# Kernel tuning notes

Hardware: AMD Instinct MI355X
Metric: run time of the kernel (lower is better)

## Reference

```python
import jax, jax.numpy as jnp
import numpy as np

N, F, E = 65536, 64, 16   # batch, fields, embedding_size
H1, H2 = 8, 4             # hidden_dims
BN_EPS = 1e-5


def setup_inputs() -> dict:
    key = jax.random.key(0)
    ks = jax.random.split(key, 12)
    rn = lambda k, shape, sc=1.0: jax.random.normal(k, shape, dtype=jnp.float32) * sc
    return {
        "Xa": rn(ks[0], (N, F)),
        "Xc": rn(ks[1], (N, F)),
        # per-field Linear(1,1) weights/biases (two first-order embedding lists)
        "w1": rn(ks[2], (F,)), "b1": rn(ks[3], (F,)),
        "w2": rn(ks[4], (F,)), "b2": rn(ks[5], (F,)),
        # per-field Linear(1,E) weights/biases (two second-order embedding lists)
        "W1": rn(ks[6], (F, E)), "B1": rn(ks[7], (F, E)),
        "W2": rn(ks[8], (F, E)), "B2": rn(ks[9], (F, E)),
        # deep MLP: linear_1 (F*E -> 8) + BN, linear_2 (8 -> 4). No final layer (init bug).
        "lin1_w": rn(ks[10], (H1, F * E), 0.01), "lin1_b": jnp.zeros((H1,), jnp.float32),
        "bn1_gamma": jnp.ones((H1,), jnp.float32), "bn1_beta": jnp.zeros((H1,), jnp.float32),
        "lin2_w": rn(ks[11], (H2, H1), 0.01), "lin2_b": jnp.full((H2,), 0.21, jnp.float32),
    }


def reference(Xa, Xc, w1, b1, w2, b2, W1, B1, W2, B2,
              lin1_w, lin1_b, bn1_gamma, bn1_beta, lin2_w, lin2_b):
    n = Xa.shape[0]
    # ---- FM first order (faithful to the torch broadcast: arr_2[i] is (N,N)
    # with entry [r,c] = Xa[r,i]*(w2[i]*Xc[c,i]+b2[i]); only mean over the
    # concat dim is consumed, so compute the column-mean analytically). ----
    first1 = (w1 * Xa + b1) * Xc                         # (N,F)
    xc_mean = jnp.mean(Xc, axis=0)                       # (F,)
    first2_cmean = Xa * (w2 * xc_mean + b2)              # (N,F) = mean over c of arr_2
    fm_first_mean = jnp.mean(first1 + first2_cmean, axis=1, keepdims=True)  # (N,1)

    # ---- FM second order: per-field (N,E) embeddings, fully batched. ----
    Xa3 = Xa[:, :, None]                                 # (N,F,1)
    Xc3 = Xc[:, :, None]
    emb = (Xa3 * W1 + B1) * Xc3 + Xa3 * (W2 * Xc3 + B2)  # (N,F,E)
    s = emb.sum(axis=1)                                  # (N,E)
    fm_second = 0.5 * (s * s - (emb * emb).sum(axis=1))  # (N,E)
    fm_second_mean = jnp.mean(fm_second, axis=1, keepdims=True)  # (N,1)

    # ---- deep part: cat of per-field (N,E) -> (N, F*E), field-major. ----
    deep = emb.reshape(n, F * E)
    h = deep @ lin1_w.T + lin1_b                         # (N,8)
    mu = h.mean(axis=0)
    var = h.var(axis=0)                                  # biased, as BN training mode
    h = (h - mu) / jnp.sqrt(var + BN_EPS) * bn1_gamma + bn1_beta
    h = jnp.tanh(h)                                      # dropout = identity (eval)
    h = h @ lin2_w.T + lin2_b                            # (N,4) — no final projection (init bug)
    deep_mean = h.mean(axis=1, keepdims=True)            # (N,1)

    return fm_first_mean + fm_second_mean + deep_mean    # (N,1)
```

## Files before the change

kernel.cpp:

```cpp
#include <hip/hip_runtime.h>
#include <math.h>

#define NROWS 65536
#define BN_EPS 1e-5f
#define MBLK   512
#define TSTR   1024

#define OFF_PARTIAL 0
#define OFF_H       65536
#define OFF_REC     589824
#define OFF_BLKT    595200
#define OFF_T       677120

__global__ __launch_bounds__(64) void precompute_kernel(
    const float* __restrict__ W1, const float* __restrict__ B1,
    const float* __restrict__ W2, const float* __restrict__ B2,
    const float* __restrict__ lin1_w, const float* __restrict__ w1,
    const float* __restrict__ b1, const float* __restrict__ b2,
    float* __restrict__ rec)
{
    int f = blockIdx.x, t = threadIdx.x;
    __shared__ float u[16], x[16], y[16];
    if (t < 16) {
        float uu = W1[f * 16 + t] + W2[f * 16 + t];
        float xx = B1[f * 16 + t];
        float yy = B2[f * 16 + t];
        u[t] = uu; x[t] = xx; y[t] = yy;
        rec[f * 84 + t]      = uu;
        rec[f * 84 + 16 + t] = xx;
        rec[f * 84 + 32 + t] = yy;
    }
    __syncthreads();
    if (t < 24) {
        int j = t & 7, which = t >> 3;
        const float* src = (which == 0) ? u : (which == 1) ? x : y;
        const float* lw = lin1_w + j * 1024 + f * 16;
        float acc = 0.f;
#pragma unroll
        for (int e = 0; e < 16; e++) acc = fmaf(src[e], lw[e], acc);
        rec[f * 84 + 48 + which * 8 + j] = acc;
    } else if (t < 30) {
        int q = t - 24;
        const float* s1 = (q == 0 || q == 3 || q == 4) ? u : (q == 1 || q == 5) ? x : y;
        const float* s2 = (q == 0) ? u : (q == 1 || q == 3) ? x : y;
        float acc = 0.f;
#pragma unroll
        for (int e = 0; e < 16; e++) acc = fmaf(s1[e], s2[e], acc);
        rec[f * 84 + 72 + q] = (q < 3 ? 1.f : 2.f) * acc;
    } else if (t == 30) {
        rec[f * 84 + 78] = w1[f];
        rec[f * 84 + 79] = b1[f];
        rec[f * 84 + 80] = b2[f];
        rec[f * 84 + 81] = 0.f;
        rec[f * 84 + 82] = 0.f;
        rec[f * 84 + 83] = 0.f;
    }
}

__global__ __launch_bounds__(256)
__attribute__((amdgpu_waves_per_eu(2, 4)))
void main_kernel(
    const float* __restrict__ Xa, const float* __restrict__ Xc,
    const float* __restrict__ rec, const float* __restrict__ lin1_b,
    float* __restrict__ ws_partial, float* __restrict__ ws_h,
    float* __restrict__ ws_blkT)
{
    __shared__ __align__(16) float smem[14848];

    int tid  = threadIdx.x;
    int lane = tid & 63;
    int wv   = tid >> 6;
    int wu   = __builtin_amdgcn_readfirstlane(wv);
    int blk  = blockIdx.x;
    int f0   = wu * 16;
    int row0 = blk * 128 + lane;
    int row1 = row0 + 64;

    {
        const float4* src = (const float4*)rec;
        float4* dst = (float4*)smem;
        for (int i = tid; i < 1344; i += 256) dst[i] = src[i];
    }

    const float4* pa0 = (const float4*)(Xa + (size_t)row0 * 64 + f0);
    const float4* pc0 = (const float4*)(Xc + (size_t)row0 * 64 + f0);
    const float4* pa1 = (const float4*)(Xa + (size_t)row1 * 64 + f0);
    const float4* pc1 = (const float4*)(Xc + (size_t)row1 * 64 + f0);
    float a_[16], c_[16], a2_[16], c2_[16];
#pragma unroll
    for (int k = 0; k < 4; k++) {
        float4 av = pa0[k], cv = pc0[k];
        a_[k * 4] = av.x; a_[k * 4 + 1] = av.y; a_[k * 4 + 2] = av.z; a_[k * 4 + 3] = av.w;
        c_[k * 4] = cv.x; c_[k * 4 + 1] = cv.y; c_[k * 4 + 2] = cv.z; c_[k * 4 + 3] = cv.w;
        float4 av2 = pa1[k], cv2 = pc1[k];
        a2_[k * 4] = av2.x; a2_[k * 4 + 1] = av2.y; a2_[k * 4 + 2] = av2.z; a2_[k * 4 + 3] = av2.w;
        c2_[k * 4] = cv2.x; c2_[k * 4 + 1] = cv2.y; c2_[k * 4 + 2] = cv2.z; c2_[k * 4 + 3] = cv2.w;
    }
    __syncthreads();

    float s[16], s2[16], hh[8], hh2[8];
#pragma unroll
    for (int e = 0; e < 16; e++) { s[e] = 0.f; s2[e] = 0.f; }
#pragma unroll
    for (int j = 0; j < 8; j++) { hh[j] = 0.f; hh2[j] = 0.f; }
    float p1_0 = 0.f, p2a_0 = 0.f, q_0 = 0.f;
    float p1_1 = 0.f, p2a_1 = 0.f, q_1 = 0.f;

    const float* recw = smem + f0 * 84;
#pragma unroll 1
    for (int i = 0; i < 16; i++) {
        const float* r = recw + i * 84;
        float a0 = a_[i],  c0 = c_[i];
        float a1 = a2_[i], c1 = c2_[i];
        float pp0 = a0 * c0, pp1 = a1 * c1;

        float rw1 = r[78], rb1 = r[79], rb2 = r[80];
        p1_0  = fmaf(fmaf(rw1, a0, rb1), c0, p1_0);
        p1_1  = fmaf(fmaf(rw1, a1, rb1), c1, p1_1);
        p2a_0 = fmaf(a0, rb2, p2a_0);
        p2a_1 = fmaf(a1, rb2, p2a_1);

        float q0 = r[72], q1 = r[73], q2 = r[74], q3 = r[75], q4 = r[76], q5 = r[77];
        q_0 = fmaf(pp0 * pp0, q0, q_0);
        q_0 = fmaf(c0 * c0,   q1, q_0);
        q_0 = fmaf(a0 * a0,   q2, q_0);
        q_0 = fmaf(pp0 * c0,  q3, q_0);
        q_0 = fmaf(pp0 * a0,  q4, q_0);
        q_0 = fmaf(pp0,       q5, q_0);
        q_1 = fmaf(pp1 * pp1, q0, q_1);
        q_1 = fmaf(c1 * c1,   q1, q_1);
        q_1 = fmaf(a1 * a1,   q2, q_1);
        q_1 = fmaf(pp1 * c1,  q3, q_1);
        q_1 = fmaf(pp1 * a1,  q4, q_1);
        q_1 = fmaf(pp1,       q5, q_1);

#pragma unroll
        for (int e = 0; e < 16; e++) {
            float u = r[e], x = r[16 + e], y = r[32 + e];
            s[e]  = fmaf(pp0, u, fmaf(c0, x, fmaf(a0, y, s[e])));
            s2[e] = fmaf(pp1, u, fmaf(c1, x, fmaf(a1, y, s2[e])));
        }
#pragma unroll
        for (int j = 0; j < 8; j++) {
            float w1c = r[48 + j], w2c = r[56 + j], w3c = r[64 + j];
            hh[j]  = fmaf(pp0, w1c, fmaf(c0, w2c, fmaf(a0, w3c, hh[j])));
            hh2[j] = fmaf(pp1, w1c, fmaf(c1, w2c, fmaf(a1, w3c, hh2[j])));
        }
    }

    {
        float cs[16];
#pragma unroll
        for (int i = 0; i < 16; i++) cs[i] = c_[i] + c2_[i];
#pragma unroll
        for (int off = 1; off < 64; off <<= 1) {
#pragma unroll
            for (int i = 0; i < 16; i++) cs[i] += __shfl_xor(cs[i], off);
        }
        if (lane == 0) {
#pragma unroll
            for (int i = 0; i < 16; i++)
                ws_blkT[(size_t)(f0 + i) * TSTR + blk] = cs[i];
        }
    }

    __syncthreads();
    {
        float* cmb0 = smem + (wv * 64 + lane) * 29;
        float* cmb1 = smem + 7424 + (wv * 64 + lane) * 29;
#pragma unroll
        for (int e = 0; e < 16; e++) { cmb0[e] = s[e]; cmb1[e] = s2[e]; }
#pragma unroll
        for (int j = 0; j < 8; j++) { cmb0[16 + j] = hh[j]; cmb1[16 + j] = hh2[j]; }
        cmb0[24] = p1_0;  cmb1[24] = p1_1;
        cmb0[25] = p2a_0; cmb1[25] = p2a_1;
        cmb0[26] = q_0;   cmb1[26] = q_1;
    }
    __syncthreads();

    if (tid < 128) {
        int set = tid >> 6;
        int l   = tid & 63;
        const float* base = smem + set * 7424;
        float S[16], H[8], P1 = 0.f, P2 = 0.f, Q = 0.f;
#pragma unroll
        for (int e = 0; e < 16; e++) S[e] = 0.f;
#pragma unroll
        for (int j = 0; j < 8; j++) H[j] = 0.f;
#pragma unroll
        for (int w = 0; w < 4; w++) {
            const float* c2 = base + (w * 64 + l) * 29;
#pragma unroll
            for (int e = 0; e < 16; e++) S[e] += c2[e];
#pragma unroll
            for (int j = 0; j < 8; j++) H[j] += c2[16 + j];
            P1 += c2[24];
            P2 += c2[25];
            Q  += c2[26];
        }
#pragma unroll
        for (int j = 0; j < 8; j++) H[j] += lin1_b[j];

        float ss = 0.f;
#pragma unroll
        for (int e = 0; e < 16; e++) ss = fmaf(S[e], S[e], ss);
        int rr = blk * 128 + set * 64 + l;
        ws_partial[rr] = (P1 + P2) * (1.f / 64.f) + (ss - Q) * (0.5f / 16.f);
        *(float4*)(ws_h + (size_t)rr * 8)     = make_float4(H[0], H[1], H[2], H[3]);
        *(float4*)(ws_h + (size_t)rr * 8 + 4) = make_float4(H[4], H[5], H[6], H[7]);

        float bn[16];
#pragma unroll
        for (int j = 0; j < 8; j++) { bn[j] = H[j]; bn[8 + j] = H[j] * H[j]; }
#pragma unroll
        for (int off = 1; off < 64; off <<= 1) {
#pragma unroll
            for (int i = 0; i < 16; i++) bn[i] += __shfl_xor(bn[i], off);
        }
        if (l == 0) {
#pragma unroll
            for (int i = 0; i < 16; i++)
                ws_blkT[(size_t)(64 + i) * TSTR + blk * 2 + set] = bn[i];
        }
    }
}

__global__ __launch_bounds__(256) void reduce_kernel(
    const float* __restrict__ ws_blkT, float* __restrict__ T)
{
    int gtid = blockIdx.x * 256 + threadIdx.x;
    int v = gtid >> 6;
    int lane = gtid & 63;
    const float* p = ws_blkT + (size_t)v * TSTR + lane;
    float acc = 0.f;
    if (v < 64) {
#pragma unroll
        for (int k = 0; k < 8; k++) acc += p[k * 64];
    } else {
#pragma unroll
        for (int k = 0; k < 16; k++) acc += p[k * 64];
    }
#pragma unroll
    for (int off = 32; off; off >>= 1) acc += __shfl_xor(acc, off);
    if (lane == 0) T[v] = acc;
}

__global__ __launch_bounds__(256) void final_kernel(
    const float* __restrict__ Xa, const float* __restrict__ w2,
    const float* __restrict__ gamma, const float* __restrict__ beta,
    const float* __restrict__ lin2_w, const float* __restrict__ lin2_b,
    const float* __restrict__ T, const float* __restrict__ ws_partial,
    const float* __restrict__ ws_h, float* __restrict__ out)
{
    __shared__ float sg[64], sScale[8], sShift[8], sColw[8];
    __shared__ float sBsum;
    int tid = threadIdx.x;
    if (tid < 64) {
        sg[tid] = w2[tid] * (T[tid] * (1.f / 65536.f));
    } else if (tid < 72) {
        int j = tid - 64;
        float mu  = T[64 + j] * (1.f / 65536.f);
        float var = T[72 + j] * (1.f / 65536.f) - mu * mu;
        float sc = gamma[j] / sqrtf(var + BN_EPS);
        sScale[j] = sc;
        sShift[j] = beta[j] - mu * sc;
    } else if (tid < 80) {
        int j = tid - 72;
        sColw[j] = lin2_w[j] + lin2_w[8 + j] + lin2_w[16 + j] + lin2_w[24 + j];
    } else if (tid == 80) {
        sBsum = lin2_b[0] + lin2_b[1] + lin2_b[2] + lin2_b[3];
    }
    __syncthreads();

    int row  = (blockIdx.x * 256 + tid) >> 1;
    int half = tid & 1;
    int fo   = half * 32;

    const float4* xa4 = (const float4*)(Xa + (size_t)row * 64 + fo);
    float p2b = 0.f;
#pragma unroll
    for (int k = 0; k < 8; k++) {
        float4 vv = xa4[k];
        int b = fo + k * 4;
        p2b += vv.x * sg[b] + vv.y * sg[b + 1] + vv.z * sg[b + 2] + vv.w * sg[b + 3];
    }

    float4 hq = *(const float4*)(ws_h + (size_t)row * 8 + half * 4);
    float hv[4] = {hq.x, hq.y, hq.z, hq.w};
    float dmp = 0.f;
#pragma unroll
    for (int jj = 0; jj < 4; jj++) {
        int j = half * 4 + jj;
        float hn = tanhf(hv[jj] * sScale[j] + sShift[j]);
        dmp = fmaf(hn, sColw[j], dmp);
    }

    float val = p2b * (1.f / 64.f) + dmp * 0.25f;
    val += __shfl_xor(val, 1);
    if (!half)
        out[row] = val + ws_partial[row] + sBsum * 0.25f;
}

extern "C" void kernel_launch(void* const* d_in, const int* in_sizes, int n_in,
                              void* d_out, int out_size, void* d_ws, size_t ws_size,
                              hipStream_t stream) {
    const float* Xa        = (const float*)d_in[0];
    const float* Xc        = (const float*)d_in[1];
    const float* w1        = (const float*)d_in[2];
    const float* b1        = (const float*)d_in[3];
    const float* w2        = (const float*)d_in[4];
    const float* b2        = (const float*)d_in[5];
    const float* W1        = (const float*)d_in[6];
    const float* B1        = (const float*)d_in[7];
    const float* W2        = (const float*)d_in[8];
    const float* B2        = (const float*)d_in[9];
    const float* lin1_w    = (const float*)d_in[10];
    const float* lin1_b    = (const float*)d_in[11];
    const float* bn1_gamma = (const float*)d_in[12];
    const float* bn1_beta  = (const float*)d_in[13];
    const float* lin2_w    = (const float*)d_in[14];
    const float* lin2_b    = (const float*)d_in[15];

    float* ws  = (float*)d_ws;
    float* out = (float*)d_out;

    float* ws_partial = ws + OFF_PARTIAL;
    float* ws_h       = ws + OFF_H;
    float* ws_rec     = ws + OFF_REC;
    float* ws_blkT    = ws + OFF_BLKT;
    float* ws_T       = ws + OFF_T;

    precompute_kernel<<<64, 64, 0, stream>>>(W1, B1, W2, B2, lin1_w,
                                             w1, b1, b2, ws_rec);
    main_kernel<<<MBLK, 256, 0, stream>>>(Xa, Xc, ws_rec, lin1_b,
                                          ws_partial, ws_h, ws_blkT);
    reduce_kernel<<<20, 256, 0, stream>>>(ws_blkT, ws_T);
    final_kernel<<<512, 256, 0, stream>>>(Xa, w2, bn1_gamma, bn1_beta,
                                          lin2_w, lin2_b, ws_T,
                                          ws_partial, ws_h, out);
}
```

Measured before the change: 124.2 us.

## Software-pipeline Xa/Xc loads across field chunks with double-buffered float4 registers

Replaces the up-front load of all 16 fields per row and the rolled loop with a fully unrolled loop in four chunks. The next chunk's float4 loads are issued while the current chunk computes, and sched_barriers keep the compiler from reordering them. The first loads are now issued before the shared-memory staging of the precomputed table, so global latency overlaps that copy. This cuts live registers from four 16-float arrays to two double buffers, but full unrolling grows code size and may change register allocation.

Result: slower. 411.5 us (+231.3%).

```diff
diff --git a/kernel.cpp b/kernel.cpp
--- a/kernel.cpp
+++ b/kernel.cpp
@@ -57,6 +57,44 @@
     }
 }
 
+#define FITER(I, AV0, CV0, AV1, CV1) do {                                   \
+    const float* r = recw + (I) * 84;    \
+    float a0 = (AV0), c0 = (CV0), a1 = (AV1), c1 = (CV1);                   \
+    float pp0 = a0 * c0, pp1 = a1 * c1;                                     \
+    float rw1 = r[78], rb1 = r[79], rb2 = r[80];                            \
+    p1_0  = fmaf(fmaf(rw1, a0, rb1), c0, p1_0);                             \
+    p1_1  = fmaf(fmaf(rw1, a1, rb1), c1, p1_1);                             \
+    p2a_0 = fmaf(a0, rb2, p2a_0);                                           \
+    p2a_1 = fmaf(a1, rb2, p2a_1);                                           \
+    float q0 = r[72], q1 = r[73], q2 = r[74];                               \
+    float q3 = r[75], q4 = r[76], q5 = r[77];                               \
+    q_0 = fmaf(pp0 * pp0, q0, q_0);  q_0 = fmaf(c0 * c0, q1, q_0);          \
+    q_0 = fmaf(a0 * a0,   q2, q_0);  q_0 = fmaf(pp0 * c0, q3, q_0);         \
+    q_0 = fmaf(pp0 * a0,  q4, q_0);  q_0 = fmaf(pp0,      q5, q_0);         \
+    q_1 = fmaf(pp1 * pp1, q0, q_1);  q_1 = fmaf(c1 * c1, q1, q_1);          \
+    q_1 = fmaf(a1 * a1,   q2, q_1);  q_1 = fmaf(pp1 * c1, q3, q_1);         \
+    q_1 = fmaf(pp1 * a1,  q4, q_1);  q_1 = fmaf(pp1,      q5, q_1);         \
+    _Pragma("unroll")                                                       \
+    for (int e = 0; e < 16; e++) {                                          \
+        float u = r[e], x = r[16 + e], y = r[32 + e];                       \
+        s[e]  = fmaf(pp0, u, fmaf(c0, x, fmaf(a0, y, s[e])));               \
+        s2[e] = fmaf(pp1, u, fmaf(c1, x, fmaf(a1, y, s2[e])));              \
+    }                                                                       \
+    _Pragma("unroll")                                                       \
+    for (int j = 0; j < 8; j++) {                                           \
+        float w1c = r[48 + j], w2c = r[56 + j], w3c = r[64 + j];            \
+        hh[j]  = fmaf(pp0, w1c, fmaf(c0, w2c, fmaf(a0, w3c, hh[j])));       \
+        hh2[j] = fmaf(pp1, w1c, fmaf(c1, w2c, fmaf(a1, w3c, hh2[j])));      \
+    }                                                                       \
+    cs[I] = c0 + c1;                                                        \
+} while (0)
+
+#define CHUNK(K, BA0, BC0, BA1, BC1)                                        \
+    FITER(4*(K)+0, BA0.x, BC0.x, BA1.x, BC1.x);                             \
+    FITER(4*(K)+1, BA0.y, BC0.y, BA1.y, BC1.y);                             \
+    FITER(4*(K)+2, BA0.z, BC0.z, BA1.z, BC1.z);                             \
+    FITER(4*(K)+3, BA0.w, BC0.w, BA1.w, BC1.w);
+
 __global__ __launch_bounds__(256)
 __attribute__((amdgpu_waves_per_eu(2, 4)))
 void main_kernel(
@@ -76,29 +114,22 @@
     int row0 = blk * 128 + lane;
     int row1 = row0 + 64;
 
+    const float4* pa0 = (const float4*)(Xa + (size_t)row0 * 64 + f0);
+    const float4* pc0 = (const float4*)(Xc + (size_t)row0 * 64 + f0);
+    const float4* pa1 = (const float4*)(Xa + (size_t)row1 * 64 + f0);
+    const float4* pc1 = (const float4*)(Xc + (size_t)row1 * 64 + f0);
+
+    float4 bA0 = pa0[0], bC0 = pc0[0], bA1 = pa1[0], bC1 = pc1[0];
+    float4 dA0 = pa0[1], dC0 = pc0[1], dA1 = pa1[1], dC1 = pc1[1];
+
     {
         const float4* src = (const float4*)rec;
         float4* dst = (float4*)smem;
         for (int i = tid; i < 1344; i += 256) dst[i] = src[i];
     }
-
-    const float4* pa0 = (const float4*)(Xa + (size_t)row0 * 64 + f0);
-    const float4* pc0 = (const float4*)(Xc + (size_t)row0 * 64 + f0);
-    const float4* pa1 = (const float4*)(Xa + (size_t)row1 * 64 + f0);
-    const float4* pc1 = (const float4*)(Xc + (size_t)row1 * 64 + f0);
-    float a_[16], c_[16], a2_[16], c2_[16];
-#pragma unroll
-    for (int k = 0; k < 4; k++) {
-        float4 av = pa0[k], cv = pc0[k];
-        a_[k * 4] = av.x; a_[k * 4 + 1] = av.y; a_[k * 4 + 2] = av.z; a_[k * 4 + 3] = av.w;
-        c_[k * 4] = cv.x; c_[k * 4 + 1] = cv.y; c_[k * 4 + 2] = cv.z; c_[k * 4 + 3] = cv.w;
-        float4 av2 = pa1[k], cv2 = pc1[k];
-        a2_[k * 4] = av2.x; a2_[k * 4 + 1] = av2.y; a2_[k * 4 + 2] = av2.z; a2_[k * 4 + 3] = av2.w;
-        c2_[k * 4] = cv2.x; c2_[k * 4 + 1] = cv2.y; c2_[k * 4 + 2] = cv2.z; c2_[k * 4 + 3] = cv2.w;
-    }
-    __syncthreads();
-
-    float s[16], s2[16], hh[8], hh2[8];
+    __syncthreads();
+
+    float s[16], s2[16], hh[8], hh2[8], cs[16];
 #pragma unroll
     for (int e = 0; e < 16; e++) { s[e] = 0.f; s2[e] = 0.f; }
 #pragma unroll
@@ -107,51 +138,18 @@
     float p1_1 = 0.f, p2a_1 = 0.f, q_1 = 0.f;
 
     const float* recw = smem + f0 * 84;
-#pragma unroll 1
-    for (int i = 0; i < 16; i++) {
-        const float* r = recw + i * 84;
-        float a0 = a_[i],  c0 = c_[i];
-        float a1 = a2_[i], c1 = c2_[i];
-        float pp0 = a0 * c0, pp1 = a1 * c1;
-
-        float rw1 = r[78], rb1 = r[79], rb2 = r[80];
-        p1_0  = fmaf(fmaf(rw1, a0, rb1), c0, p1_0);
-        p1_1  = fmaf(fmaf(rw1, a1, rb1), c1, p1_1);
-        p2a_0 = fmaf(a0, rb2, p2a_0);
-        p2a_1 = fmaf(a1, rb2, p2a_1);
-
-        float q0 = r[72], q1 = r[73], q2 = r[74], q3 = r[75], q4 = r[76], q5 = r[77];
-        q_0 = fmaf(pp0 * pp0, q0, q_0);
-        q_0 = fmaf(c0 * c0,   q1, q_0);
-        q_0 = fmaf(a0 * a0,   q2, q_0);
-        q_0 = fmaf(pp0 * c0,  q3, q_0);
-        q_0 = fmaf(pp0 * a0,  q4, q_0);
-        q_0 = fmaf(pp0,       q5, q_0);
-        q_1 = fmaf(pp1 * pp1, q0, q_1);
-        q_1 = fmaf(c1 * c1,   q1, q_1);
-        q_1 = fmaf(a1 * a1,   q2, q_1);
-        q_1 = fmaf(pp1 * c1,  q3, q_1);
-        q_1 = fmaf(pp1 * a1,  q4, q_1);
-        q_1 = fmaf(pp1,       q5, q_1);
-
-#pragma unroll
-        for (int e = 0; e < 16; e++) {
-            float u = r[e], x = r[16 + e], y = r[32 + e];
-            s[e]  = fmaf(pp0, u, fmaf(c0, x, fmaf(a0, y, s[e])));
-            s2[e] = fmaf(pp1, u, fmaf(c1, x, fmaf(a1, y, s2[e])));
-        }
-#pragma unroll
-        for (int j = 0; j < 8; j++) {
-            float w1c = r[48 + j], w2c = r[56 + j], w3c = r[64 + j];
-            hh[j]  = fmaf(pp0, w1c, fmaf(c0, w2c, fmaf(a0, w3c, hh[j])));
-            hh2[j] = fmaf(pp1, w1c, fmaf(c1, w2c, fmaf(a1, w3c, hh2[j])));
-        }
-    }
+
+    CHUNK(0, bA0, bC0, bA1, bC1);
+    __builtin_amdgcn_sched_barrier(0);
+    bA0 = pa0[2]; bC0 = pc0[2]; bA1 = pa1[2]; bC1 = pc1[2];
+    CHUNK(1, dA0, dC0, dA1, dC1);
+    __builtin_amdgcn_sched_barrier(0);
+    dA0 = pa0[3]; dC0 = pc0[3]; dA1 = pa1[3]; dC1 = pc1[3];
+    CHUNK(2, bA0, bC0, bA1, bC1);
+    __builtin_amdgcn_sched_barrier(0);
+    CHUNK(3, dA0, dC0, dA1, dC1);
 
     {
-        float cs[16];
-#pragma unroll
-        for (int i = 0; i < 16; i++) cs[i] = c_[i] + c2_[i];
 #pragma unroll
         for (int off = 1; off < 64; off <<= 1) {
 #pragma unroll
```

## Fuse main, reduce and final kernels with software grid barriers

Applied to the files above, without the earlier changes.

Merges the main, reduce and final kernels into one persistent kernel that uses an atomic-counter grid barrier, held in workspace and reset by the precompute kernel. Per-row partials and hidden activations now stay in registers instead of going to global workspace. The final pass no longer re-reads Xa; it reuses values already in registers. Shared memory is halved by processing the two row sets one after the other. This removes two launches and the extra global traffic, but relies on all 512 blocks being resident at once and adds spin-wait barrier cost.

New measurement: 236.5 us. 1.9x slower.

```diff
diff --git a/kernel.cpp b/kernel.cpp
--- a/kernel.cpp
+++ b/kernel.cpp
@@ -6,18 +6,17 @@
 #define MBLK   512
 #define TSTR   1024
 
-#define OFF_PARTIAL 0
-#define OFF_H       65536
-#define OFF_REC     589824
-#define OFF_BLKT    595200
-#define OFF_T       677120
+#define OFF_REC   589824
+#define OFF_BLKT  595200
+#define OFF_T     677120
+#define OFF_CNT   677216
 
 __global__ __launch_bounds__(64) void precompute_kernel(
     const float* __restrict__ W1, const float* __restrict__ B1,
     const float* __restrict__ W2, const float* __restrict__ B2,
     const float* __restrict__ lin1_w, const float* __restrict__ w1,
     const float* __restrict__ b1, const float* __restrict__ b2,
-    float* __restrict__ rec)
+    float* __restrict__ rec, unsigned* __restrict__ cnt)
 {
     int f = blockIdx.x, t = threadIdx.x;
     __shared__ float u[16], x[16], y[16];
@@ -54,18 +53,36 @@
         rec[f * 84 + 81] = 0.f;
         rec[f * 84 + 82] = 0.f;
         rec[f * 84 + 83] = 0.f;
-    }
+    } else if (t == 31 && f == 0) {
+        *cnt = 0u;
+    }
+}
+
+__device__ __forceinline__ void grid_barrier(unsigned* cnt, unsigned target)
+{
+    __syncthreads();
+    if (threadIdx.x == 0) {
+        __hip_atomic_fetch_add(cnt, 1u, __ATOMIC_ACQ_REL, __HIP_MEMORY_SCOPE_AGENT);
+        while (__hip_atomic_load(cnt, __ATOMIC_ACQUIRE, __HIP_MEMORY_SCOPE_AGENT) < target) {
+            __builtin_amdgcn_s_sleep(2);
+        }
+    }
+    __syncthreads();
+    __threadfence();
 }
 
 __global__ __launch_bounds__(256)
 __attribute__((amdgpu_waves_per_eu(2, 4)))
-void main_kernel(
+void fused_kernel(
     const float* __restrict__ Xa, const float* __restrict__ Xc,
     const float* __restrict__ rec, const float* __restrict__ lin1_b,
-    float* __restrict__ ws_partial, float* __restrict__ ws_h,
-    float* __restrict__ ws_blkT)
+    const float* __restrict__ w2, const float* __restrict__ gamma,
+    const float* __restrict__ beta, const float* __restrict__ lin2_w,
+    const float* __restrict__ lin2_b,
+    float* __restrict__ ws_blkT, float* __restrict__ ws_T,
+    unsigned* __restrict__ cnt, float* __restrict__ out)
 {
-    __shared__ __align__(16) float smem[14848];
+    __shared__ __align__(16) float smem[7424];
 
     int tid  = threadIdx.x;
     int lane = tid & 63;
@@ -166,30 +183,30 @@
 
     __syncthreads();
     {
-        float* cmb0 = smem + (wv * 64 + lane) * 29;
-        float* cmb1 = smem + 7424 + (wv * 64 + lane) * 29;
-#pragma unroll
-        for (int e = 0; e < 16; e++) { cmb0[e] = s[e]; cmb1[e] = s2[e]; }
-#pragma unroll
-        for (int j = 0; j < 8; j++) { cmb0[16 + j] = hh[j]; cmb1[16 + j] = hh2[j]; }
-        cmb0[24] = p1_0;  cmb1[24] = p1_1;
-        cmb0[25] = p2a_0; cmb1[25] = p2a_1;
-        cmb0[26] = q_0;   cmb1[26] = q_1;
-    }
-    __syncthreads();
-
-    if (tid < 128) {
-        int set = tid >> 6;
-        int l   = tid & 63;
-        const float* base = smem + set * 7424;
-        float S[16], H[8], P1 = 0.f, P2 = 0.f, Q = 0.f;
+        float* cmb = smem + (wv * 64 + lane) * 29;
+#pragma unroll
+        for (int e = 0; e < 16; e++) cmb[e] = s[e];
+#pragma unroll
+        for (int j = 0; j < 8; j++) cmb[16 + j] = hh[j];
+        cmb[24] = p1_0;
+        cmb[25] = p2a_0;
+        cmb[26] = q_0;
+    }
+    __syncthreads();
+
+    float H[8];
+    float rowPartial = 0.f;
+    int l_ = tid & 63;
+
+    if (tid < 64) {
+        float S[16], P1 = 0.f, P2 = 0.f, Q = 0.f;
 #pragma unroll
         for (int e = 0; e < 16; e++) S[e] = 0.f;
 #pragma unroll
         for (int j = 0; j < 8; j++) H[j] = 0.f;
 #pragma unroll
         for (int w = 0; w < 4; w++) {
-            const float* c2 = base + (w * 64 + l) * 29;
+            const float* c2 = smem + (w * 64 + l_) * 29;
 #pragma unroll
             for (int e = 0; e < 16; e++) S[e] += c2[e];
 #pragma unroll
@@ -200,14 +217,10 @@
         }
 #pragma unroll
         for (int j = 0; j < 8; j++) H[j] += lin1_b[j];
-
         float ss = 0.f;
 #pragma unroll
         for (int e = 0; e < 16; e++) ss = fmaf(S[e], S[e], ss);
-        int rr = blk * 128 + set * 64 + l;
-        ws_partial[rr] = (P1 + P2) * (1.f / 64.f) + (ss - Q) * (0.5f / 16.f);
-        *(float4*)(ws_h + (size_t)rr * 8)     = make_float4(H[0], H[1], H[2], H[3]);
-        *(float4*)(ws_h + (size_t)rr * 8 + 4) = make_float4(H[4], H[5], H[6], H[7]);
+        rowPartial = (P1 + P2) * (1.f / 64.f) + (ss - Q) * (0.5f / 16.f);
 
         float bn[16];
 #pragma unroll
@@ -217,88 +230,130 @@
 #pragma unroll
             for (int i = 0; i < 16; i++) bn[i] += __shfl_xor(bn[i], off);
         }
-        if (l == 0) {
+        if (l_ == 0) {
 #pragma unroll
             for (int i = 0; i < 16; i++)
-                ws_blkT[(size_t)(64 + i) * TSTR + blk * 2 + set] = bn[i];
-        }
-    }
-}
-
-__global__ __launch_bounds__(256) void reduce_kernel(
-    const float* __restrict__ ws_blkT, float* __restrict__ T)
-{
-    int gtid = blockIdx.x * 256 + threadIdx.x;
-    int v = gtid >> 6;
-    int lane = gtid & 63;
-    const float* p = ws_blkT + (size_t)v * TSTR + lane;
-    float acc = 0.f;
-    if (v < 64) {
-#pragma unroll
-        for (int k = 0; k < 8; k++) acc += p[k * 64];
-    } else {
-#pragma unroll
-        for (int k = 0; k < 16; k++) acc += p[k * 64];
-    }
-#pragma unroll
-    for (int off = 32; off; off >>= 1) acc += __shfl_xor(acc, off);
-    if (lane == 0) T[v] = acc;
-}
-
-__global__ __launch_bounds__(256) void final_kernel(
-    const float* __restrict__ Xa, const float* __restrict__ w2,
-    const float* __restrict__ gamma, const float* __restrict__ beta,
-    const float* __restrict__ lin2_w, const float* __restrict__ lin2_b,
-    const float* __restrict__ T, const float* __restrict__ ws_partial,
-    const float* __restrict__ ws_h, float* __restrict__ out)
-{
-    __shared__ float sg[64], sScale[8], sShift[8], sColw[8];
-    __shared__ float sBsum;
-    int tid = threadIdx.x;
+                ws_blkT[(size_t)(64 + i) * TSTR + blk * 2] = bn[i];
+        }
+    }
+    __syncthreads();
+
+    {
+        float* cmb = smem + (wv * 64 + lane) * 29;
+#pragma unroll
+        for (int e = 0; e < 16; e++) cmb[e] = s2[e];
+#pragma unroll
+        for (int j = 0; j < 8; j++) cmb[16 + j] = hh2[j];
+        cmb[24] = p1_1;
+        cmb[25] = p2a_1;
+        cmb[26] = q_1;
+    }
+    __syncthreads();
+
+    if (tid >= 64 && tid < 128) {
+        float S[16], P1 = 0.f, P2 = 0.f, Q = 0.f;
+#pragma unroll
+        for (int e = 0; e < 16; e++) S[e] = 0.f;
+#pragma unroll
+        for (int j = 0; j < 8; j++) H[j] = 0.f;
+#pragma unroll
+        for (int w = 0; w < 4; w++) {
+            const float* c2 = smem + (w * 64 + l_) * 29;
+#pragma unroll
+            for (int e = 0; e < 16; e++) S[e] += c2[e];
+#pragma unroll
+            for (int j = 0; j < 8; j++) H[j] += c2[16 + j];
+            P1 += c2[24];
+            P2 += c2[25];
+            Q  += c2[26];
+        }
+#pragma unroll
+        for (int j = 0; j < 8; j++) H[j] += lin1_b[j];
+        float ss = 0.f;
+#pragma unroll
+        for (int e = 0; e < 16; e++) ss = fmaf(S[e], S[e], ss);
+        rowPartial = (P1 + P2) * (1.f / 64.f) + (ss - Q) * (0.5f / 16.f);
+
+        float bn[16];
+#pragma unroll
+        for (int j = 0; j < 8; j++) { bn[j] = H[j]; bn[8 + j] = H[j] * H[j]; }
+#pragma unroll
+        for (int off = 1; off < 64; off <<= 1) {
+#pragma unroll
+            for (int i = 0; i < 16; i++) bn[i] += __shfl_xor(bn[i], off);
+        }
+        if (l_ == 0) {
+#pragma unroll
+            for (int i = 0; i < 16; i++)
+                ws_blkT[(size_t)(64 + i) * TSTR + blk * 2 + 1] = bn[i];
+        }
+    }
+
+    grid_barrier(cnt, MBLK);
+    if (blk < 20) {
+        int gtid = blk * 256 + tid;
+        int v  = gtid >> 6;
+        int ln = gtid & 63;
+        const float* p = ws_blkT + (size_t)v * TSTR + ln;
+        float acc = 0.f;
+        if (v < 64) {
+#pragma unroll
+            for (int k = 0; k < 8; k++) acc += p[k * 64];
+        } else {
+#pragma unroll
+            for (int k = 0; k < 16; k++) acc += p[k * 64];
+        }
+#pragma unroll
+        for (int off = 32; off; off >>= 1) acc += __shfl_xor(acc, off);
+        if (ln == 0) ws_T[v] = acc;
+    }
+    grid_barrier(cnt, 2 * MBLK);
+
     if (tid < 64) {
-        sg[tid] = w2[tid] * (T[tid] * (1.f / 65536.f));
+        smem[tid] = w2[tid] * (ws_T[tid] * (1.f / 65536.f));
     } else if (tid < 72) {
         int j = tid - 64;
-        float mu  = T[64 + j] * (1.f / 65536.f);
-        float var = T[72 + j] * (1.f / 65536.f) - mu * mu;
+        float mu  = ws_T[64 + j] * (1.f / 65536.f);
+        float var = ws_T[72 + j] * (1.f / 65536.f) - mu * mu;
         float sc = gamma[j] / sqrtf(var + BN_EPS);
-        sScale[j] = sc;
-        sShift[j] = beta[j] - mu * sc;
+        smem[64 + j] = sc;
+        smem[72 + j] = beta[j] - mu * sc;
     } else if (tid < 80) {
         int j = tid - 72;
-        sColw[j] = lin2_w[j] + lin2_w[8 + j] + lin2_w[16 + j] + lin2_w[24 + j];
+        smem[80 + j] = lin2_w[j] + lin2_w[8 + j] + lin2_w[16 + j] + lin2_w[24 + j];
     } else if (tid == 80) {
-        sBsum = lin2_b[0] + lin2_b[1] + lin2_b[2] + lin2_b[3];
-    }
-    __syncthreads();
-
-    int row  = (blockIdx.x * 256 + tid) >> 1;
-    int half = tid & 1;
-    int fo   = half * 32;
-
-    const float4* xa4 = (const float4*)(Xa + (size_t)row * 64 + fo);
-    float p2b = 0.f;
-#pragma unroll
-    for (int k = 0; k < 8; k++) {
-        float4 vv = xa4[k];
-        int b = fo + k * 4;
-        p2b += vv.x * sg[b] + vv.y * sg[b + 1] + vv.z * sg[b + 2] + vv.w * sg[b + 3];
-    }
-
-    float4 hq = *(const float4*)(ws_h + (size_t)row * 8 + half * 4);
-    float hv[4] = {hq.x, hq.y, hq.z, hq.w};
-    float dmp = 0.f;
-#pragma unroll
-    for (int jj = 0; jj < 4; jj++) {
-        int j = half * 4 + jj;
-        float hn = tanhf(hv[jj] * sScale[j] + sShift[j]);
-        dmp = fmaf(hn, sColw[j], dmp);
-    }
-
-    float val = p2b * (1.f / 64.f) + dmp * 0.25f;
-    val += __shfl_xor(val, 1);
-    if (!half)
-        out[row] = val + ws_partial[row] + sBsum * 0.25f;
+        smem[88] = lin2_b[0] + lin2_b[1] + lin2_b[2] + lin2_b[3];
+    }
+    __syncthreads();
+
+    {
+        float qd0 = 0.f, qd1 = 0.f;
+#pragma unroll
+        for (int i = 0; i < 16; i++) {
+            float sgv = smem[f0 + i];
+            qd0 = fmaf(a_[i],  sgv, qd0);
+            qd1 = fmaf(a2_[i], sgv, qd1);
+        }
+        smem[96 + (wv * 64 + lane) * 2]     = qd0;
+        smem[96 + (wv * 64 + lane) * 2 + 1] = qd1;
+    }
+    __syncthreads();
+
+    if (tid < 128) {
+        int set_ = tid >> 6;
+        float p2b = 0.f;
+#pragma unroll
+        for (int w = 0; w < 4; w++)
+            p2b += smem[96 + (w * 64 + l_) * 2 + set_];
+        float dmp = 0.f;
+#pragma unroll
+        for (int j = 0; j < 8; j++) {
+            float hn = tanhf(H[j] * smem[64 + j] + smem[72 + j]);
+            dmp = fmaf(hn, smem[80 + j], dmp);
+        }
+        int rr = blk * 128 + tid;
+        out[rr] = p2b * (1.f / 64.f) + dmp * 0.25f + rowPartial + smem[88] * 0.25f;
+    }
 }
 
 extern "C" void kernel_launch(void* const* d_in, const int* in_sizes, int n_in,
@@ -324,18 +379,15 @@
     float* ws  = (float*)d_ws;
     float* out = (float*)d_out;
 
-    float* ws_partial = ws + OFF_PARTIAL;
-    float* ws_h       = ws + OFF_H;
-    float* ws_rec     = ws + OFF_REC;
-    float* ws_blkT    = ws + OFF_BLKT;
-    float* ws_T       = ws + OFF_T;
+    float*    ws_rec  = ws + OFF_REC;
+    float*    ws_blkT = ws + OFF_BLKT;
+    float*    ws_T    = ws + OFF_T;
+    unsigned* ws_cnt  = (unsigned*)(ws + OFF_CNT);
 
     precompute_kernel<<<64, 64, 0, stream>>>(W1, B1, W2, B2, lin1_w,
-                                             w1, b1, b2, ws_rec);
-    main_kernel<<<MBLK, 256, 0, stream>>>(Xa, Xc, ws_rec, lin1_b,
-                                          ws_partial, ws_h, ws_blkT);
-    reduce_kernel<<<20, 256, 0, stream>>>(ws_blkT, ws_T);
-    final_kernel<<<512, 256, 0, stream>>>(Xa, w2, bn1_gamma, bn1_beta,
-                                          lin2_w, lin2_b, ws_T,
-                                          ws_partial, ws_h, out);
+                                             w1, b1, b2, ws_rec, ws_cnt);
+    fused_kernel<<<MBLK, 256, 0, stream>>>(Xa, Xc, ws_rec, lin1_b,
+                                           w2, bn1_gamma, bn1_beta,
+                                           lin2_w, lin2_b,
+                                           ws_blkT, ws_T, ws_cnt, out);
 }
```
